# Kernel tuning notes

Measured on AMD Instinct MI355X. Metric: run time of the kernel, lower is better.

The kernel has to match this reference:

```python
import jax, jax.numpy as jnp
import numpy as np

# Static multi-scale feature map shapes (H_l, W_l)
SHAPES = ((112, 112), (56, 56), (28, 28))
D_MODEL, D_HEAD, N_HEADS, N_LEVELS, N_POINTS = 256, 64, 6, 3, 9


def setup_inputs() -> dict:
    key = jax.random.key(0)
    ks = jax.random.split(key, 14)
    N, Lq = 4, 2048
    Lin = sum(h * w for h, w in SHAPES)  # 16464
    s = 0.02  # weight init scale
    return {
        "tgt": jax.random.normal(ks[0], (N, Lq, D_MODEL), jnp.float32),
        "src": jax.random.normal(ks[1], (N, Lin, D_MODEL), jnp.float32),
        "query_pos": jax.random.normal(ks[2], (N, Lq, D_MODEL), jnp.float32),
        "reference_points": jax.random.uniform(ks[3], (N, Lq, N_LEVELS, 2), jnp.float32),
        "src_spatial_shapes": jnp.array(SHAPES, jnp.int32),
        "level_start_index": jnp.array([0, 112 * 112, 112 * 112 + 56 * 56], jnp.int32),
        "src_padding_mask": jnp.zeros((N, Lin), bool),
        "W_off": jax.random.normal(ks[4], (D_MODEL, N_HEADS * N_LEVELS * N_POINTS * 2), jnp.float32) * s,
        "b_off": jax.random.normal(ks[5], (N_HEADS * N_LEVELS * N_POINTS * 2,), jnp.float32) * 0.5,
        "W_attn": jax.random.normal(ks[6], (D_MODEL, N_HEADS * N_LEVELS * N_POINTS), jnp.float32) * s,
        "b_attn": jax.random.normal(ks[7], (N_HEADS * N_LEVELS * N_POINTS,), jnp.float32) * s,
        "W_val": jax.random.normal(ks[8], (D_MODEL, N_HEADS * D_HEAD), jnp.float32) * s,
        "b_val": jnp.zeros((N_HEADS * D_HEAD,), jnp.float32),
        "W_out": jax.random.normal(ks[9], (N_HEADS * D_HEAD, D_MODEL), jnp.float32) * s,
        "b_out": jnp.zeros((D_MODEL,), jnp.float32),
    }


def _bilinear_sample(v, loc, H_l, W_l):
    """v: (N, Hh, H_l*W_l, d) level values; loc: (N, Lq, Hh, P, 2) in [0,1].
    grid_sample(align_corners=False, padding_mode='zeros') equivalent.
    Returns (N, Hh, Lq, P, d)."""
    N, Hh, _, d = v.shape
    Lq, P = loc.shape[1], loc.shape[3]
    x = loc[..., 0] * W_l - 0.5  # (N, Lq, Hh, P)
    y = loc[..., 1] * H_l - 0.5
    x0 = jnp.floor(x)
    y0 = jnp.floor(y)
    wx1 = x - x0
    wy1 = y - y0
    wx0 = 1.0 - wx1
    wy0 = 1.0 - wy1
    x0i = x0.astype(jnp.int32)
    y0i = y0.astype(jnp.int32)

    def gather(xi, yi, w):
        inb = (xi >= 0) & (xi < W_l) & (yi >= 0) & (yi < H_l)
        xc = jnp.clip(xi, 0, W_l - 1)
        yc = jnp.clip(yi, 0, H_l - 1)
        idx = (yc * W_l + xc).transpose(0, 2, 1, 3).reshape(N, Hh, Lq * P)
        g = jnp.take_along_axis(v, idx[..., None], axis=2)  # (N, Hh, Lq*P, d)
        w_eff = (w * inb).transpose(0, 2, 1, 3).reshape(N, Hh, Lq * P, 1)
        return g * w_eff

    out = (gather(x0i, y0i, wx0 * wy0)
           + gather(x0i + 1, y0i, wx1 * wy0)
           + gather(x0i, y0i + 1, wx0 * wy1)
           + gather(x0i + 1, y0i + 1, wx1 * wy1))
    return out.reshape(N, Hh, Lq, P, d)


def reference(tgt, src, query_pos, reference_points, src_spatial_shapes,
              level_start_index, src_padding_mask, W_off, b_off, W_attn, b_attn,
              W_val, b_val, W_out, b_out):
    N, Lq, _ = tgt.shape
    Hh, d, L, P = N_HEADS, D_HEAD, N_LEVELS, N_POINTS
    q = tgt + query_pos  # with_pos_embed

    value = src @ W_val + b_val
    value = jnp.where(src_padding_mask[..., None], 0.0, value)
    value = value.reshape(N, -1, Hh, d).transpose(0, 2, 1, 3)  # (N, Hh, Lin, d)

    off = (q @ W_off + b_off).reshape(N, Lq, Hh, L, P, 2)
    attn = jax.nn.softmax((q @ W_attn + b_attn).reshape(N, Lq, Hh, L * P), axis=-1)
    attn = attn.reshape(N, Lq, Hh, L, P)

    # offset_normalizer = (W_l, H_l); loc in normalized [0,1] coordinates
    norm = jnp.array([[w, h] for h, w in SHAPES], dtype=q.dtype)  # (L, 2)
    loc = reference_points[:, :, None, :, None, :] + off / norm[None, None, None, :, None, :]

    out = jnp.zeros((N, Hh, Lq, d), dtype=q.dtype)
    start = 0
    for l, (H_l, W_l) in enumerate(SHAPES):
        v_l = value[:, :, start:start + H_l * W_l]
        sampled = _bilinear_sample(v_l, loc[:, :, :, l], H_l, W_l)  # (N, Hh, Lq, P, d)
        out = out + jnp.einsum('nhqpd,nqhp->nhqd', sampled, attn[:, :, :, l])
        start += H_l * W_l

    out = out.transpose(0, 2, 1, 3).reshape(N, Lq, Hh * d)
    return out @ W_out + b_out  # dropout = identity in eval mode
```

## Files before the change

kernel.cpp:

```cpp
#include <hip/hip_runtime.h>
#include <math.h>

#define NB 4
#define LQ 2048
#define DM 256
#define HH 6
#define DH 64
#define LIN 16464
#define LINP 16512
#define NOA 512
#define NVAL 384

typedef unsigned short ushort_t;
typedef unsigned int uint_t;
typedef __attribute__((ext_vector_type(8))) short s8v;
typedef __attribute__((ext_vector_type(4))) float f4v;

__device__ __forceinline__ ushort_t f2bf(float f) {
  union { float f; unsigned u; } v; v.f = f;
  unsigned r = v.u + 0x7fffu + ((v.u >> 16) & 1u);
  return (ushort_t)(r >> 16);
}

typedef __attribute__((address_space(3))) char lds_char_t;
typedef const __attribute__((address_space(1))) char glb_char_t;
__device__ __forceinline__ void gload16(const void* g, void* l) {
  __builtin_amdgcn_global_load_lds((glb_char_t*)g, (lds_char_t*)l, 16, 0, 0);
}

__global__ __launch_bounds__(256)
void prep_k(const float4* __restrict__ tgt, const float4* __restrict__ qpos,
            ushort4* __restrict__ q_bf,
            const float4* __restrict__ src, ushort4* __restrict__ src_bf,
            const float* __restrict__ W_val, ushort_t* __restrict__ bt_val,
            const float* __restrict__ W_off, const float* __restrict__ W_attn,
            ushort_t* __restrict__ bt_oa,
            const float* __restrict__ W_out, ushort_t* __restrict__ bt_out,
            const float* __restrict__ b_off, const float* __restrict__ b_attn,
            float* __restrict__ bias_oa) {
  const int blk = blockIdx.x, tid = threadIdx.x;
  if (blk < 2048) {
    const int i = blk * 256 + tid;
    float4 x = tgt[i], y = qpos[i];
    ushort4 r;
    r.x = f2bf(x.x + y.x); r.y = f2bf(x.y + y.y);
    r.z = f2bf(x.z + y.z); r.w = f2bf(x.w + y.w);
    q_bf[i] = r;
  } else if (blk < 18560) {
    const int ib = blk - 2048;
    const int b = ib / 4128;
    const int idx = (ib - b * 4128) * 256 + tid;
    const int r = idx >> 6, kq = idx & 63;
    ushort4 o;
    if (r < LIN) {
      float4 x = src[(size_t)(b * LIN + r) * 64 + kq];
      o.x = f2bf(x.x); o.y = f2bf(x.y); o.z = f2bf(x.z); o.w = f2bf(x.w);
    } else {
      o.x = o.y = o.z = o.w = 0;
    }
    src_bf[(size_t)(b * LINP + r) * 64 + kq] = o;
  } else {
    const int i = (blk - 18560) * 256 + tid;
    if (i < 98304) {
      const int n = i >> 8, k = i & 255;
      bt_val[i] = f2bf(W_val[(size_t)k * 384 + n]);
    } else if (i < 229376) {
      const int j = i - 98304;
      const int n = j >> 8, k = j & 255;
      float v = 0.f;
      if (n < 324) v = W_off[(size_t)k * 324 + n];
      else if (n < 486) v = W_attn[(size_t)k * 162 + (n - 324)];
      bt_oa[j] = f2bf(v);
    } else if (i < 327680) {
      const int j = i - 229376;
      const int n = j / 384, k = j - n * 384;
      bt_out[j] = f2bf(W_out[(size_t)k * 256 + n]);
    } else {
      const int j = i - 327680;
      if (j < 512) bias_oa[j] = (j < 324) ? b_off[j] : (j < 486 ? b_attn[j - 324] : 0.f);
    }
  }
}

template <int MODE, int NBX, int NBY, int CPX>
__global__ __launch_bounds__(256)
void mfma_gemm_k(const ushort_t* __restrict__ Act, const ushort_t* __restrict__ Wt,
                 const float* __restrict__ bias, void* __restrict__ Cout,
                 int N, int K) {
  __shared__ char lds[3][16384];
  const int bid = blockIdx.x;
  const int r = (bid & 7) * CPX + (bid >> 3);
  if (r >= NBX * NBY) return;
  const int bx = r / NBY, by = r - bx * NBY;
  const int m0 = bx * 128, n0 = by * 128;

  const int t = threadIdx.x;
  const int lane = t & 63, wid = t >> 6;
  const int wr = wid >> 1, wc = wid & 1;
  const int l15 = lane & 15, kg = lane >> 4;
  const int nk = K >> 5;

  const int srow = lane >> 2;
  const int koct = (lane & 3) ^ ((lane >> 3) & 3);
  const int rsw = (l15 >> 1) & 3;

  const size_t WA0 = (size_t)(n0 + wid * 16 + srow) * K + koct * 8;
  const size_t WA1 = WA0 + (size_t)64 * K;
  const size_t XB0 = (size_t)(m0 + wid * 16 + srow) * K + koct * 8;
  const size_t XB1 = XB0 + (size_t)64 * K;

  f4v acc[4][4];
#pragma unroll
  for (int i = 0; i < 4; ++i)
#pragma unroll
    for (int j = 0; j < 4; ++j) acc[i][j] = (f4v){0.f, 0.f, 0.f, 0.f};

#define STAGE(ks_)                                                       \
  { char* d_ = &lds[(ks_) % 3][0]; const int ko_ = (ks_) << 5;           \
    gload16(Wt + WA0 + ko_,  d_ + wid * 1024);                           \
    gload16(Wt + WA1 + ko_,  d_ + 4096 + wid * 1024);                    \
    gload16(Act + XB0 + ko_, d_ + 8192 + wid * 1024);                    \
    gload16(Act + XB1 + ko_, d_ + 12288 + wid * 1024); }

  STAGE(0);
  STAGE(1);

  for (int ks = 0; ks < nk; ++ks) {
    if (ks + 1 < nk) {
      asm volatile("s_waitcnt vmcnt(4)" ::: "memory");
    } else {
      asm volatile("s_waitcnt vmcnt(0)" ::: "memory");
    }
    __builtin_amdgcn_s_barrier();
    asm volatile("" ::: "memory");
    if (ks + 2 < nk) STAGE(ks + 2);

    const char* d = &lds[ks % 3][0];
    s8v av[4], bv[4];
#pragma unroll
    for (int mr = 0; mr < 4; ++mr)
      av[mr] = *(const s8v*)(d + (wr * 64 + mr * 16 + l15) * 64 + ((kg ^ rsw) << 4));
#pragma unroll
    for (int nr = 0; nr < 4; ++nr)
      bv[nr] = *(const s8v*)(d + 8192 + (wc * 64 + nr * 16 + l15) * 64 + ((kg ^ rsw) << 4));
#pragma unroll
    for (int mr = 0; mr < 4; ++mr)
#pragma unroll
      for (int nr = 0; nr < 4; ++nr)
        acc[mr][nr] = __builtin_amdgcn_mfma_f32_16x16x32_bf16(av[mr], bv[nr],
                                                              acc[mr][nr], 0, 0, 0);
  }
#undef STAGE

  if (MODE == 0) {
#pragma unroll
    for (int mr = 0; mr < 4; ++mr) {
      const int ch = n0 + wr * 64 + mr * 16 + kg * 4;
      const float4 b4 = *(const float4*)(bias + ch);
#pragma unroll
      for (int nr = 0; nr < 4; ++nr) {
        const int qrow = m0 + wc * 64 + nr * 16 + l15;
        float4 v;
        v.x = acc[mr][nr][0] + b4.x;
        v.y = acc[mr][nr][1] + b4.y;
        v.z = acc[mr][nr][2] + b4.z;
        v.w = acc[mr][nr][3] + b4.w;
        *(float4*)((float*)Cout + (size_t)qrow * N + ch) = v;
      }
    }
  } else {
    const int bq = bx / 129;
    const int rb = (bx - bq * 129) * 128;
#pragma unroll
    for (int mr = 0; mr < 4; ++mr) {
      const int ch = n0 + wr * 64 + mr * 16 + kg * 4;
      const int h = ch >> 6, dd = ch & 63;
      const float4 b4 = *(const float4*)(bias + ch);
      ushort_t* obase = (ushort_t*)Cout + (size_t)(bq * HH + h) * LIN * DH + dd;
#pragma unroll
      for (int nr = 0; nr < 4; ++nr) {
        const int ii = rb + wc * 64 + nr * 16 + l15;
        if (ii < LIN) {
          ushort4 o;
          o.x = f2bf(acc[mr][nr][0] + b4.x);
          o.y = f2bf(acc[mr][nr][1] + b4.y);
          o.z = f2bf(acc[mr][nr][2] + b4.z);
          o.w = f2bf(acc[mr][nr][3] + b4.w);
          *(ushort4*)(obase + (size_t)ii * DH) = o;
        }
      }
    }
  }
}

__global__ __launch_bounds__(256)
void deform_sample_k(const ushort_t* __restrict__ value,
                     const float* __restrict__ oa,
                     const float* __restrict__ refp,
                     uint_t* __restrict__ otmp) {
  __shared__ int4 sp[4][56];
  const int lane = threadIdx.x & 63, wv = threadIdx.x >> 6;
  const int wid = blockIdx.x * 4 + wv;
  const int s = wid >> 11;
  const int qq = wid & 2047;
  const int nb = s / HH, h = s - nb * HH;
  const int nq = nb * LQ + qq;

  float lg = -INFINITY;
  if (lane < 27) lg = oa[(size_t)nq * NOA + 324 + h * 27 + lane];
  float mx = lg;
#pragma unroll
  for (int m = 1; m < 64; m <<= 1) mx = fmaxf(mx, __shfl_xor(mx, m, 64));
  float e = (lane < 27) ? __expf(lg - mx) : 0.f;
  float ssum = e;
#pragma unroll
  for (int m = 1; m < 64; m <<= 1) ssum += __shfl_xor(ssum, m, 64);

  if (lane < 27) {
    const float aw = e / ssum;
    const int lvl = (lane >= 18) ? 2 : (lane >= 9 ? 1 : 0);
    const float Wf = (lvl == 0) ? 112.f : (lvl == 1 ? 56.f : 28.f);
    const int Wi = (lvl == 0) ? 112 : (lvl == 1 ? 56 : 28);
    const int base = (lvl == 0) ? 0 : (lvl == 1 ? 12544 : 15680);
    const float2 rp = *(const float2*)(refp + (size_t)nq * 6 + lvl * 2);
    const float2 of = *(const float2*)(oa + (size_t)nq * NOA + h * 54 + lane * 2);
    const float x = rp.x * Wf + of.x - 0.5f;
    const float y = rp.y * Wf + of.y - 0.5f;
    const float x0f = floorf(x), y0f = floorf(y);
    const float wx1 = x - x0f, wy1 = y - y0f;
    const float wx0 = 1.f - wx1, wy0 = 1.f - wy1;
    const int x0 = (int)x0f, y0 = (int)y0f;
    const int x1 = x0 + 1, y1 = y0 + 1;
    const bool bx0 = (x0 >= 0) & (x0 < Wi), bx1 = (x1 >= 0) & (x1 < Wi);
    const bool by0 = (y0 >= 0) & (y0 < Wi), by1 = (y1 >= 0) & (y1 < Wi);
    const int a00 = (bx0 & by0) ? ((base + y0 * Wi + x0) << 7) : 0;
    const int a01 = (bx1 & by0) ? ((base + y0 * Wi + x1) << 7) : 0;
    const int a10 = (bx0 & by1) ? ((base + y1 * Wi + x0) << 7) : 0;
    const int a11 = (bx1 & by1) ? ((base + y1 * Wi + x1) << 7) : 0;
    const float w00 = (bx0 & by0) ? aw * wx0 * wy0 : 0.f;
    const float w01 = (bx1 & by0) ? aw * wx1 * wy0 : 0.f;
    const float w10 = (bx0 & by1) ? aw * wx0 * wy1 : 0.f;
    const float w11 = (bx1 & by1) ? aw * wx1 * wy1 : 0.f;
    sp[wv][lane * 2 + 0] = make_int4(a00, __float_as_int(w00), a01, __float_as_int(w01));
    sp[wv][lane * 2 + 1] = make_int4(a10, __float_as_int(w10), a11, __float_as_int(w11));
  } else if (lane == 27) {
    sp[wv][54] = make_int4(0, 0, 0, 0);
    sp[wv][55] = make_int4(0, 0, 0, 0);
  }
  __syncthreads();

  const uint_t slice = (uint_t)__builtin_amdgcn_readfirstlane(s);
  const char* vbase = (const char*)value + (size_t)slice * (LIN * DH * 2);
  const int j4 = (lane & 31) * 4;
  const int half = lane >> 5;
  float a0 = 0.f, a1 = 0.f;
#pragma unroll 2
  for (int i = 0; i < 14; ++i) {
    const int pt = half * 14 + i;
    const int4 c01 = sp[wv][pt * 2];
    const int4 c23 = sp[wv][pt * 2 + 1];
    const uint_t u0 = *(const uint_t*)(vbase + (uint_t)(c01.x + j4));
    const uint_t u1 = *(const uint_t*)(vbase + (uint_t)(c01.z + j4));
    const uint_t u2 = *(const uint_t*)(vbase + (uint_t)(c23.x + j4));
    const uint_t u3 = *(const uint_t*)(vbase + (uint_t)(c23.z + j4));
    const float w0 = __int_as_float(c01.y), w1 = __int_as_float(c01.w);
    const float w2 = __int_as_float(c23.y), w3 = __int_as_float(c23.w);
    a0 += w0 * __uint_as_float(u0 << 16);
    a1 += w0 * __uint_as_float(u0 & 0xffff0000u);
    a0 += w1 * __uint_as_float(u1 << 16);
    a1 += w1 * __uint_as_float(u1 & 0xffff0000u);
    a0 += w2 * __uint_as_float(u2 << 16);
    a1 += w2 * __uint_as_float(u2 & 0xffff0000u);
    a0 += w3 * __uint_as_float(u3 << 16);
    a1 += w3 * __uint_as_float(u3 & 0xffff0000u);
  }
  a0 += __shfl_xor(a0, 32, 64);
  a1 += __shfl_xor(a1, 32, 64);
  if (lane < 32) {
    const uint_t packed = (uint_t)f2bf(a0) | ((uint_t)f2bf(a1) << 16);
    otmp[(size_t)nq * 192 + h * 32 + lane] = packed;
  }
}

extern "C" void kernel_launch(void* const* d_in, const int* in_sizes, int n_in,
                              void* d_out, int out_size, void* d_ws, size_t ws_size,
                              hipStream_t stream) {
  const float* tgt   = (const float*)d_in[0];
  const float* src   = (const float*)d_in[1];
  const float* qpos  = (const float*)d_in[2];
  const float* refp  = (const float*)d_in[3];
  const float* W_off  = (const float*)d_in[7];
  const float* b_off  = (const float*)d_in[8];
  const float* W_attn = (const float*)d_in[9];
  const float* b_attn = (const float*)d_in[10];
  const float* W_val  = (const float*)d_in[11];
  const float* b_val  = (const float*)d_in[12];
  const float* W_out  = (const float*)d_in[13];
  const float* b_out  = (const float*)d_in[14];

  char* ws = (char*)d_ws;
  ushort_t* src_bf  = (ushort_t*)(ws);
  uint_t*   otmp    = (uint_t*)  (ws);
  ushort_t* q_bf    = (ushort_t*)(ws + 33816576);
  ushort_t* val_bf  = (ushort_t*)(ws + 38010880);
  float*    oa      = (float*)   (ws + 88588288);
  ushort_t* bt_val  = (ushort_t*)(ws + 105365504);
  ushort_t* bt_oa   = (ushort_t*)(ws + 105562112);
  ushort_t* bt_out  = (ushort_t*)(ws + 105824256);
  float*    bias_oa = (float*)   (ws + 106020864);

  prep_k<<<19842, 256, 0, stream>>>((const float4*)tgt, (const float4*)qpos,
                                    (ushort4*)q_bf, (const float4*)src,
                                    (ushort4*)src_bf, W_val, bt_val,
                                    W_off, W_attn, bt_oa, W_out, bt_out,
                                    b_off, b_attn, bias_oa);

  mfma_gemm_k<1, 516, 3, 194><<<1552, 256, 0, stream>>>(
      src_bf, bt_val, b_val, val_bf, NVAL, DM);
  mfma_gemm_k<0, 64, 4, 32><<<256, 256, 0, stream>>>(
      q_bf, bt_oa, bias_oa, oa, NOA, DM);

  deform_sample_k<<<12288, 256, 0, stream>>>(val_bf, oa, refp, otmp);

  mfma_gemm_k<0, 64, 2, 16><<<128, 256, 0, stream>>>(
      (const ushort_t*)otmp, bt_out, b_out, (float*)d_out, DM, NVAL);
}
```

Baseline: 118.8 us.

## Enlarge GEMM tiles to 256x128 with 8 waves and widen sampler loads

The MFMA GEMM moves from 128x128 tiles on 4 waves to 256x128 tiles on 8 waves (512 threads). Each weight tile is now shared across more activation rows, so fewer blocks launch. Source padding and workspace offsets are adjusted to the new 256-row granularity. The deformable sampler now has each lane load 8 bytes (4 bf16 channels) per corner, with 4 point groups reduced by two shuffles, instead of 4-byte loads split into two halves. The larger tiles mean fewer blocks for the small GEMMs (64 and 128 blocks), which risks underusing the CUs.

Result: slower. 133.0 us (+12.0%).

```diff
diff --git a/kernel.cpp b/kernel.cpp
--- a/kernel.cpp
+++ b/kernel.cpp
@@ -7,7 +7,7 @@
 #define HH 6
 #define DH 64
 #define LIN 16464
-#define LINP 16512
+#define LINP 16640
 #define NOA 512
 #define NVAL 384
 
@@ -46,10 +46,10 @@
     r.x = f2bf(x.x + y.x); r.y = f2bf(x.y + y.y);
     r.z = f2bf(x.z + y.z); r.w = f2bf(x.w + y.w);
     q_bf[i] = r;
-  } else if (blk < 18560) {
+  } else if (blk < 18688) {
     const int ib = blk - 2048;
-    const int b = ib / 4128;
-    const int idx = (ib - b * 4128) * 256 + tid;
+    const int b = ib / 4160;
+    const int idx = (ib - b * 4160) * 256 + tid;
     const int r = idx >> 6, kq = idx & 63;
     ushort4 o;
     if (r < LIN) {
@@ -60,7 +60,7 @@
     }
     src_bf[(size_t)(b * LINP + r) * 64 + kq] = o;
   } else {
-    const int i = (blk - 18560) * 256 + tid;
+    const int i = (blk - 18688) * 256 + tid;
     if (i < 98304) {
       const int n = i >> 8, k = i & 255;
       bt_val[i] = f2bf(W_val[(size_t)k * 384 + n]);
@@ -83,20 +83,20 @@
 }
 
 template <int MODE, int NBX, int NBY, int CPX>
-__global__ __launch_bounds__(256)
+__global__ __launch_bounds__(512)
 void mfma_gemm_k(const ushort_t* __restrict__ Act, const ushort_t* __restrict__ Wt,
                  const float* __restrict__ bias, void* __restrict__ Cout,
                  int N, int K) {
-  __shared__ char lds[3][16384];
+  __shared__ char lds[3][24576];
   const int bid = blockIdx.x;
   const int r = (bid & 7) * CPX + (bid >> 3);
   if (r >= NBX * NBY) return;
   const int bx = r / NBY, by = r - bx * NBY;
-  const int m0 = bx * 128, n0 = by * 128;
+  const int m0 = bx * 256, n0 = by * 128;
 
   const int t = threadIdx.x;
   const int lane = t & 63, wid = t >> 6;
-  const int wr = wid >> 1, wc = wid & 1;
+  const int wr = wid >> 2, wc = wid & 3;
   const int l15 = lane & 15, kg = lane >> 4;
   const int nk = K >> 5;
 
@@ -104,10 +104,9 @@
   const int koct = (lane & 3) ^ ((lane >> 3) & 3);
   const int rsw = (l15 >> 1) & 3;
 
-  const size_t WA0 = (size_t)(n0 + wid * 16 + srow) * K + koct * 8;
-  const size_t WA1 = WA0 + (size_t)64 * K;
-  const size_t XB0 = (size_t)(m0 + wid * 16 + srow) * K + koct * 8;
-  const size_t XB1 = XB0 + (size_t)64 * K;
+  const size_t WS  = (size_t)(n0 + wid * 16 + srow) * K + koct * 8;
+  const size_t AS0 = (size_t)(m0 + wid * 32 + srow) * K + koct * 8;
+  const size_t AS1 = AS0 + (size_t)16 * K;
 
   f4v acc[4][4];
 #pragma unroll
@@ -117,17 +116,16 @@
 
 #define STAGE(ks_)                                                       \
   { char* d_ = &lds[(ks_) % 3][0]; const int ko_ = (ks_) << 5;           \
-    gload16(Wt + WA0 + ko_,  d_ + wid * 1024);                           \
-    gload16(Wt + WA1 + ko_,  d_ + 4096 + wid * 1024);                    \
-    gload16(Act + XB0 + ko_, d_ + 8192 + wid * 1024);                    \
-    gload16(Act + XB1 + ko_, d_ + 12288 + wid * 1024); }
+    gload16(Wt + WS + ko_,   d_ + wid * 1024);                           \
+    gload16(Act + AS0 + ko_, d_ + 8192 + wid * 2048);                    \
+    gload16(Act + AS1 + ko_, d_ + 8192 + wid * 2048 + 1024); }
 
   STAGE(0);
   STAGE(1);
 
   for (int ks = 0; ks < nk; ++ks) {
     if (ks + 1 < nk) {
-      asm volatile("s_waitcnt vmcnt(4)" ::: "memory");
+      asm volatile("s_waitcnt vmcnt(3)" ::: "memory");
     } else {
       asm volatile("s_waitcnt vmcnt(0)" ::: "memory");
     }
@@ -169,8 +167,8 @@
       }
     }
   } else {
-    const int bq = bx / 129;
-    const int rb = (bx - bq * 129) * 128;
+    const int bq = bx / 65;
+    const int rb = (bx - bq * 65) * 256;
 #pragma unroll
     for (int mr = 0; mr < 4; ++mr) {
       const int ch = n0 + wr * 64 + mr * 16 + kg * 4;
@@ -251,34 +249,38 @@
 
   const uint_t slice = (uint_t)__builtin_amdgcn_readfirstlane(s);
   const char* vbase = (const char*)value + (size_t)slice * (LIN * DH * 2);
-  const int j4 = (lane & 31) * 4;
-  const int half = lane >> 5;
-  float a0 = 0.f, a1 = 0.f;
-#pragma unroll 2
-  for (int i = 0; i < 14; ++i) {
-    const int pt = half * 14 + i;
+  const int g = lane >> 4, lgx = lane & 15;
+  const int boff = lgx * 8;
+  float a0 = 0.f, a1 = 0.f, a2 = 0.f, a3 = 0.f;
+#pragma unroll
+  for (int i = 0; i < 7; ++i) {
+    const int pt = g + i * 4;
     const int4 c01 = sp[wv][pt * 2];
     const int4 c23 = sp[wv][pt * 2 + 1];
-    const uint_t u0 = *(const uint_t*)(vbase + (uint_t)(c01.x + j4));
-    const uint_t u1 = *(const uint_t*)(vbase + (uint_t)(c01.z + j4));
-    const uint_t u2 = *(const uint_t*)(vbase + (uint_t)(c23.x + j4));
-    const uint_t u3 = *(const uint_t*)(vbase + (uint_t)(c23.z + j4));
-    const float w0 = __int_as_float(c01.y), w1 = __int_as_float(c01.w);
-    const float w2 = __int_as_float(c23.y), w3 = __int_as_float(c23.w);
-    a0 += w0 * __uint_as_float(u0 << 16);
-    a1 += w0 * __uint_as_float(u0 & 0xffff0000u);
-    a0 += w1 * __uint_as_float(u1 << 16);
-    a1 += w1 * __uint_as_float(u1 & 0xffff0000u);
-    a0 += w2 * __uint_as_float(u2 << 16);
-    a1 += w2 * __uint_as_float(u2 & 0xffff0000u);
-    a0 += w3 * __uint_as_float(u3 << 16);
-    a1 += w3 * __uint_as_float(u3 & 0xffff0000u);
-  }
-  a0 += __shfl_xor(a0, 32, 64);
-  a1 += __shfl_xor(a1, 32, 64);
-  if (lane < 32) {
-    const uint_t packed = (uint_t)f2bf(a0) | ((uint_t)f2bf(a1) << 16);
-    otmp[(size_t)nq * 192 + h * 32 + lane] = packed;
+#define CORNER(ADDR, WBITS)                                              \
+    {                                                                    \
+      const uint2 u = *(const uint2*)(vbase + (uint_t)((ADDR) + boff));  \
+      const float w = __int_as_float(WBITS);                             \
+      a0 += w * __uint_as_float(u.x << 16);                              \
+      a1 += w * __uint_as_float(u.x & 0xffff0000u);                      \
+      a2 += w * __uint_as_float(u.y << 16);                              \
+      a3 += w * __uint_as_float(u.y & 0xffff0000u);                      \
+    }
+    CORNER(c01.x, c01.y);
+    CORNER(c01.z, c01.w);
+    CORNER(c23.x, c23.y);
+    CORNER(c23.z, c23.w);
+#undef CORNER
+  }
+  a0 += __shfl_xor(a0, 16, 64); a1 += __shfl_xor(a1, 16, 64);
+  a2 += __shfl_xor(a2, 16, 64); a3 += __shfl_xor(a3, 16, 64);
+  a0 += __shfl_xor(a0, 32, 64); a1 += __shfl_xor(a1, 32, 64);
+  a2 += __shfl_xor(a2, 32, 64); a3 += __shfl_xor(a3, 32, 64);
+  if (lane < 16) {
+    uint2 p;
+    p.x = (uint_t)f2bf(a0) | ((uint_t)f2bf(a1) << 16);
+    p.y = (uint_t)f2bf(a2) | ((uint_t)f2bf(a3) << 16);
+    ((uint2*)otmp)[(size_t)nq * 96 + h * 16 + lgx] = p;
   }
 }
 
@@ -301,27 +303,27 @@
   char* ws = (char*)d_ws;
   ushort_t* src_bf  = (ushort_t*)(ws);
   uint_t*   otmp    = (uint_t*)  (ws);
-  ushort_t* q_bf    = (ushort_t*)(ws + 33816576);
-  ushort_t* val_bf  = (ushort_t*)(ws + 38010880);
-  float*    oa      = (float*)   (ws + 88588288);
-  ushort_t* bt_val  = (ushort_t*)(ws + 105365504);
-  ushort_t* bt_oa   = (ushort_t*)(ws + 105562112);
-  ushort_t* bt_out  = (ushort_t*)(ws + 105824256);
-  float*    bias_oa = (float*)   (ws + 106020864);
-
-  prep_k<<<19842, 256, 0, stream>>>((const float4*)tgt, (const float4*)qpos,
+  ushort_t* q_bf    = (ushort_t*)(ws + 34078720);
+  ushort_t* val_bf  = (ushort_t*)(ws + 38273024);
+  float*    oa      = (float*)   (ws + 88850432);
+  ushort_t* bt_val  = (ushort_t*)(ws + 105627648);
+  ushort_t* bt_oa   = (ushort_t*)(ws + 105824256);
+  ushort_t* bt_out  = (ushort_t*)(ws + 106086400);
+  float*    bias_oa = (float*)   (ws + 106283008);
+
+  prep_k<<<19970, 256, 0, stream>>>((const float4*)tgt, (const float4*)qpos,
                                     (ushort4*)q_bf, (const float4*)src,
                                     (ushort4*)src_bf, W_val, bt_val,
                                     W_off, W_attn, bt_oa, W_out, bt_out,
                                     b_off, b_attn, bias_oa);
 
-  mfma_gemm_k<1, 516, 3, 194><<<1552, 256, 0, stream>>>(
+  mfma_gemm_k<1, 260, 3, 98><<<784, 512, 0, stream>>>(
       src_bf, bt_val, b_val, val_bf, NVAL, DM);
-  mfma_gemm_k<0, 64, 4, 32><<<256, 256, 0, stream>>>(
+  mfma_gemm_k<0, 32, 4, 16><<<128, 512, 0, stream>>>(
       q_bf, bt_oa, bias_oa, oa, NOA, DM);
 
   deform_sample_k<<<12288, 256, 0, stream>>>(val_bf, oa, refp, otmp);
 
-  mfma_gemm_k<0, 64, 2, 16><<<128, 256, 0, stream>>>(
+  mfma_gemm_k<0, 32, 2, 8><<<64, 512, 0, stream>>>(
       (const ushort_t*)otmp, bt_out, b_out, (float*)d_out, DM, NVAL);
 }
```

## Fuse fp32-to-bf16 src conversion into the value-projection GEMM loader

Applied to the files above, without the earlier changes.

Removes the separate pass in prep_k that converted src to a padded bf16 buffer. A new GEMM kernel reads fp32 src straight from global memory into registers, packs it to bf16 with v_cvt_pk_bf16_f32, and writes it into LDS, while the weights still stream in through global_load_lds. This drops a full write and re-read of a ~34MB intermediate. The cost is register-staged activation loads and software pipelining with manual vmcnt waits, which may leave less latency hiding than the direct LDS loads.

Measured after the change: 112.3 us. 1.06x faster.

```diff
diff --git a/kernel.cpp b/kernel.cpp
--- a/kernel.cpp
+++ b/kernel.cpp
@@ -7,7 +7,6 @@
 #define HH 6
 #define DH 64
 #define LIN 16464
-#define LINP 16512
 #define NOA 512
 #define NVAL 384
 
@@ -22,6 +21,12 @@
   return (ushort_t)(r >> 16);
 }
 
+__device__ __forceinline__ uint_t cvtpk(float lo, float hi) {
+  uint_t r;
+  asm("v_cvt_pk_bf16_f32 %0, %1, %2" : "=v"(r) : "v"(lo), "v"(hi));
+  return r;
+}
+
 typedef __attribute__((address_space(3))) char lds_char_t;
 typedef const __attribute__((address_space(1))) char glb_char_t;
 __device__ __forceinline__ void gload16(const void* g, void* l) {
@@ -31,7 +36,6 @@
 __global__ __launch_bounds__(256)
 void prep_k(const float4* __restrict__ tgt, const float4* __restrict__ qpos,
             ushort4* __restrict__ q_bf,
-            const float4* __restrict__ src, ushort4* __restrict__ src_bf,
             const float* __restrict__ W_val, ushort_t* __restrict__ bt_val,
             const float* __restrict__ W_off, const float* __restrict__ W_attn,
             ushort_t* __restrict__ bt_oa,
@@ -46,21 +50,8 @@
     r.x = f2bf(x.x + y.x); r.y = f2bf(x.y + y.y);
     r.z = f2bf(x.z + y.z); r.w = f2bf(x.w + y.w);
     q_bf[i] = r;
-  } else if (blk < 18560) {
-    const int ib = blk - 2048;
-    const int b = ib / 4128;
-    const int idx = (ib - b * 4128) * 256 + tid;
-    const int r = idx >> 6, kq = idx & 63;
-    ushort4 o;
-    if (r < LIN) {
-      float4 x = src[(size_t)(b * LIN + r) * 64 + kq];
-      o.x = f2bf(x.x); o.y = f2bf(x.y); o.z = f2bf(x.z); o.w = f2bf(x.w);
-    } else {
-      o.x = o.y = o.z = o.w = 0;
-    }
-    src_bf[(size_t)(b * LINP + r) * 64 + kq] = o;
   } else {
-    const int i = (blk - 18560) * 256 + tid;
+    const int i = (blk - 2048) * 256 + tid;
     if (i < 98304) {
       const int n = i >> 8, k = i & 255;
       bt_val[i] = f2bf(W_val[(size_t)k * 384 + n]);
@@ -82,10 +73,135 @@
   }
 }
 
-template <int MODE, int NBX, int NBY, int CPX>
+template <int NBX, int NBY, int CPX>
+__global__ __launch_bounds__(256)
+void mfma_gemm_vsrc_k(const float* __restrict__ Src, const ushort_t* __restrict__ Wt,
+                      const float* __restrict__ bias, ushort_t* __restrict__ Cout) {
+  __shared__ char lds[3][16384];
+  const int bid = blockIdx.x;
+  const int r = (bid & 7) * CPX + (bid >> 3);
+  if (r >= NBX * NBY) return;
+  const int bx = r / NBY, by = r - bx * NBY;
+  const int bq = bx / 129;
+  const int rb = (bx - bq * 129) * 128;
+  const int n0 = by * 128;
+
+  const int t = threadIdx.x;
+  const int lane = t & 63, wid = t >> 6;
+  const int wr = wid >> 1, wc = wid & 1;
+  const int l15 = lane & 15, kg = lane >> 4;
+
+  const int srow = lane >> 2;
+  const int koct = (lane & 3) ^ ((lane >> 3) & 3);
+  const int rsw = (l15 >> 1) & 3;
+  const size_t WS0 = (size_t)(n0 + wid * 16 + srow) * DM + koct * 8;
+  const size_t WS1 = WS0 + (size_t)64 * DM;
+
+  const int ar = t >> 1, aj = t & 1;
+  const int asw = ((ar & 15) >> 1) & 3;
+  const int o0 = (2 * aj) ^ asw, o1 = (2 * aj + 1) ^ asw;
+  const int arow_l = (rb + ar < LIN) ? (rb + ar) : (LIN - 1);
+  const float* abase = Src + (size_t)(bq * LIN + arow_l) * DM;
+  char* const aw0 = (char*)&lds[0][0];
+
+  f4v acc[4][4];
+#pragma unroll
+  for (int i = 0; i < 4; ++i)
+#pragma unroll
+    for (int j = 0; j < 4; ++j) acc[i][j] = (f4v){0.f, 0.f, 0.f, 0.f};
+
+  float4 ld[4];
+
+#define ACT_LOAD(ks_)                                                    \
+  { const int kb_ = (ks_) << 5;                                          \
+    ld[0] = *(const float4*)(abase + kb_ + o0 * 8);                      \
+    ld[1] = *(const float4*)(abase + kb_ + o0 * 8 + 4);                  \
+    ld[2] = *(const float4*)(abase + kb_ + o1 * 8);                      \
+    ld[3] = *(const float4*)(abase + kb_ + o1 * 8 + 4); }
+
+#define ACT_WRITE(ks_)                                                  \
+  { char* d_ = &lds[(ks_) % 3][8192] + ar * 64 + aj * 32;               \
+    uint4 c0, c1;                                                       \
+    c0.x = cvtpk(ld[0].x, ld[0].y); c0.y = cvtpk(ld[0].z, ld[0].w);     \
+    c0.z = cvtpk(ld[1].x, ld[1].y); c0.w = cvtpk(ld[1].z, ld[1].w);     \
+    c1.x = cvtpk(ld[2].x, ld[2].y); c1.y = cvtpk(ld[2].z, ld[2].w);     \
+    c1.z = cvtpk(ld[3].x, ld[3].y); c1.w = cvtpk(ld[3].z, ld[3].w);     \
+    *(uint4*)(d_) = c0;                                                 \
+    *(uint4*)(d_ + 16) = c1; }
+
+#define GLOADW(ks_)                                                     \
+  { char* d_ = &lds[(ks_) % 3][0]; const int ko_ = (ks_) << 5;          \
+    gload16(Wt + WS0 + ko_, d_ + wid * 1024);                           \
+    gload16(Wt + WS1 + ko_, d_ + 4096 + wid * 1024); }
+
+  ACT_LOAD(0);
+  GLOADW(0);
+  asm volatile("s_waitcnt vmcnt(2)" ::: "memory");
+  ACT_WRITE(0);
+  ACT_LOAD(1);
+  GLOADW(1);
+  asm volatile("s_waitcnt vmcnt(2)" ::: "memory");
+  ACT_WRITE(1);
+
+  const int nk = DM >> 5;
+  for (int ks = 0; ks < nk; ++ks) {
+    if (ks + 2 < nk) ACT_LOAD(ks + 2);
+    if (ks == nk - 1) asm volatile("s_waitcnt vmcnt(0)" ::: "memory");
+    asm volatile("s_waitcnt lgkmcnt(0)" ::: "memory");
+    __builtin_amdgcn_s_barrier();
+    asm volatile("" ::: "memory");
+    if (ks + 2 < nk) GLOADW(ks + 2);
+
+    const char* d = &lds[ks % 3][0];
+    s8v av[4], bv[4];
+#pragma unroll
+    for (int mr = 0; mr < 4; ++mr)
+      av[mr] = *(const s8v*)(d + (wr * 64 + mr * 16 + l15) * 64 + ((kg ^ rsw) << 4));
+#pragma unroll
+    for (int nr = 0; nr < 4; ++nr)
+      bv[nr] = *(const s8v*)(d + 8192 + (wc * 64 + nr * 16 + l15) * 64 + ((kg ^ rsw) << 4));
+#pragma unroll
+    for (int mr = 0; mr < 4; ++mr)
+#pragma unroll
+      for (int nr = 0; nr < 4; ++nr)
+        acc[mr][nr] = __builtin_amdgcn_mfma_f32_16x16x32_bf16(av[mr], bv[nr],
+                                                              acc[mr][nr], 0, 0, 0);
+
+    if (ks + 2 < nk) {
+      asm volatile("s_waitcnt vmcnt(2)" ::: "memory");
+      ACT_WRITE(ks + 2);
+    }
+  }
+#undef ACT_LOAD
+#undef ACT_WRITE
+#undef GLOADW
+
+#pragma unroll
+  for (int mr = 0; mr < 4; ++mr) {
+    const int ch = n0 + wr * 64 + mr * 16 + kg * 4;
+    const int h = ch >> 6, dd = ch & 63;
+    const float4 b4 = *(const float4*)(bias + ch);
+    ushort_t* obase = Cout + (size_t)(bq * HH + h) * LIN * DH + dd;
+#pragma unroll
+    for (int nr = 0; nr < 4; ++nr) {
+      const int ii = rb + wc * 64 + nr * 16 + l15;
+      if (ii < LIN) {
+        ushort4 o;
+        o.x = f2bf(acc[mr][nr][0] + b4.x);
+        o.y = f2bf(acc[mr][nr][1] + b4.y);
+        o.z = f2bf(acc[mr][nr][2] + b4.z);
+        o.w = f2bf(acc[mr][nr][3] + b4.w);
+        *(ushort4*)(obase + (size_t)ii * DH) = o;
+      }
+    }
+  }
+  (void)aw0;
+}
+
+template <int NBX, int NBY, int CPX>
 __global__ __launch_bounds__(256)
 void mfma_gemm_k(const ushort_t* __restrict__ Act, const ushort_t* __restrict__ Wt,
-                 const float* __restrict__ bias, void* __restrict__ Cout,
+                 const float* __restrict__ bias, float* __restrict__ Cout,
                  int N, int K) {
   __shared__ char lds[3][16384];
   const int bid = blockIdx.x;
@@ -152,43 +268,19 @@
   }
 #undef STAGE
 
-  if (MODE == 0) {
-#pragma unroll
-    for (int mr = 0; mr < 4; ++mr) {
-      const int ch = n0 + wr * 64 + mr * 16 + kg * 4;
-      const float4 b4 = *(const float4*)(bias + ch);
-#pragma unroll
-      for (int nr = 0; nr < 4; ++nr) {
-        const int qrow = m0 + wc * 64 + nr * 16 + l15;
-        float4 v;
-        v.x = acc[mr][nr][0] + b4.x;
-        v.y = acc[mr][nr][1] + b4.y;
-        v.z = acc[mr][nr][2] + b4.z;
-        v.w = acc[mr][nr][3] + b4.w;
-        *(float4*)((float*)Cout + (size_t)qrow * N + ch) = v;
-      }
-    }
-  } else {
-    const int bq = bx / 129;
-    const int rb = (bx - bq * 129) * 128;
-#pragma unroll
-    for (int mr = 0; mr < 4; ++mr) {
-      const int ch = n0 + wr * 64 + mr * 16 + kg * 4;
-      const int h = ch >> 6, dd = ch & 63;
-      const float4 b4 = *(const float4*)(bias + ch);
-      ushort_t* obase = (ushort_t*)Cout + (size_t)(bq * HH + h) * LIN * DH + dd;
-#pragma unroll
-      for (int nr = 0; nr < 4; ++nr) {
-        const int ii = rb + wc * 64 + nr * 16 + l15;
-        if (ii < LIN) {
-          ushort4 o;
-          o.x = f2bf(acc[mr][nr][0] + b4.x);
-          o.y = f2bf(acc[mr][nr][1] + b4.y);
-          o.z = f2bf(acc[mr][nr][2] + b4.z);
-          o.w = f2bf(acc[mr][nr][3] + b4.w);
-          *(ushort4*)(obase + (size_t)ii * DH) = o;
-        }
-      }
+#pragma unroll
+  for (int mr = 0; mr < 4; ++mr) {
+    const int ch = n0 + wr * 64 + mr * 16 + kg * 4;
+    const float4 b4 = *(const float4*)(bias + ch);
+#pragma unroll
+    for (int nr = 0; nr < 4; ++nr) {
+      const int qrow = m0 + wc * 64 + nr * 16 + l15;
+      float4 v;
+      v.x = acc[mr][nr][0] + b4.x;
+      v.y = acc[mr][nr][1] + b4.y;
+      v.z = acc[mr][nr][2] + b4.z;
+      v.w = acc[mr][nr][3] + b4.w;
+      *(float4*)(Cout + (size_t)qrow * N + ch) = v;
     }
   }
 }
@@ -299,29 +391,27 @@
   const float* b_out  = (const float*)d_in[14];
 
   char* ws = (char*)d_ws;
-  ushort_t* src_bf  = (ushort_t*)(ws);
-  uint_t*   otmp    = (uint_t*)  (ws);
-  ushort_t* q_bf    = (ushort_t*)(ws + 33816576);
-  ushort_t* val_bf  = (ushort_t*)(ws + 38010880);
-  float*    oa      = (float*)   (ws + 88588288);
-  ushort_t* bt_val  = (ushort_t*)(ws + 105365504);
-  ushort_t* bt_oa   = (ushort_t*)(ws + 105562112);
-  ushort_t* bt_out  = (ushort_t*)(ws + 105824256);
-  float*    bias_oa = (float*)   (ws + 106020864);
-
-  prep_k<<<19842, 256, 0, stream>>>((const float4*)tgt, (const float4*)qpos,
-                                    (ushort4*)q_bf, (const float4*)src,
-                                    (ushort4*)src_bf, W_val, bt_val,
-                                    W_off, W_attn, bt_oa, W_out, bt_out,
-                                    b_off, b_attn, bias_oa);
-
-  mfma_gemm_k<1, 516, 3, 194><<<1552, 256, 0, stream>>>(
-      src_bf, bt_val, b_val, val_bf, NVAL, DM);
-  mfma_gemm_k<0, 64, 4, 32><<<256, 256, 0, stream>>>(
+  ushort_t* val_bf  = (ushort_t*)(ws);
+  float*    oa      = (float*)   (ws + 50577408);
+  ushort_t* q_bf    = (ushort_t*)(ws + 67354624);
+  uint_t*   otmp    = (uint_t*)  (ws + 71548928);
+  ushort_t* bt_val  = (ushort_t*)(ws + 77840384);
+  ushort_t* bt_oa   = (ushort_t*)(ws + 78036992);
+  ushort_t* bt_out  = (ushort_t*)(ws + 78299136);
+  float*    bias_oa = (float*)   (ws + 78495744);
+
+  prep_k<<<3330, 256, 0, stream>>>((const float4*)tgt, (const float4*)qpos,
+                                   (ushort4*)q_bf, W_val, bt_val,
+                                   W_off, W_attn, bt_oa, W_out, bt_out,
+                                   b_off, b_attn, bias_oa);
+
+  mfma_gemm_vsrc_k<516, 3, 194><<<1552, 256, 0, stream>>>(
+      src, bt_val, b_val, val_bf);
+  mfma_gemm_k<64, 4, 32><<<256, 256, 0, stream>>>(
       q_bf, bt_oa, bias_oa, oa, NOA, DM);
 
   deform_sample_k<<<12288, 256, 0, stream>>>(val_bf, oa, refp, otmp);
 
-  mfma_gemm_k<0, 64, 2, 16><<<128, 256, 0, stream>>>(
+  mfma_gemm_k<64, 2, 16><<<128, 256, 0, stream>>>(
       (const ushort_t*)otmp, bt_out, b_out, (float*)d_out, DM, NVAL);
 }
```
